# Kernel tuning notes

Hardware: AMD Instinct MI355X
Metric: run time of the kernel (lower is better)

## Reference

```python
import jax, jax.numpy as jnp
import numpy as np

EMBED_DIM = 1024
NUM_HEADS = 16
HEAD_DIM = EMBED_DIM // NUM_HEADS
SCALE = float(np.sqrt(HEAD_DIM))


def setup_inputs() -> dict:
    key = jax.random.key(0)
    ks = jax.random.split(key, 5)
    B, S, D = 4, 2048, EMBED_DIM
    lim_qkv = 1.0 / np.sqrt(D)
    lim_out = 1.0 / np.sqrt(D)
    return {
        "x": jax.random.normal(ks[0], (B, S, D), dtype=jnp.float32),
        "qkv_w": jax.random.uniform(ks[1], (3 * D, D), jnp.float32, -lim_qkv, lim_qkv),
        "qkv_b": jax.random.uniform(ks[2], (3 * D,), jnp.float32, -lim_qkv, lim_qkv),
        "out_w": jax.random.uniform(ks[3], (D, D), jnp.float32, -lim_out, lim_out),
        "out_b": jax.random.uniform(ks[4], (D,), jnp.float32, -lim_out, lim_out),
    }


def reference(x, qkv_w, qkv_b, out_w, out_b):
    B, S, D = x.shape
    H, Hd = NUM_HEADS, HEAD_DIM
    # qkv projection (torch Linear: x @ W.T + b)
    qkv = x @ qkv_w.T + qkv_b                      # [B, S, 3D]
    qkv = qkv.reshape(B, S, 3, H, Hd)
    q = jnp.transpose(qkv[:, :, 0], (0, 2, 1, 3))  # [B, H, S, Hd]
    k = jnp.transpose(qkv[:, :, 1], (0, 2, 1, 3))
    v = jnp.transpose(qkv[:, :, 2], (0, 2, 1, 3))
    attn = jnp.einsum("bhqd,bhkd->bhqk", q, k) / SCALE  # [B, H, S, S]
    attn = jax.nn.softmax(attn, axis=-1)
    out = jnp.einsum("bhqk,bhkd->bhqd", attn, v)        # [B, H, S, Hd]
    out = jnp.transpose(out, (0, 2, 1, 3)).reshape(B, S, D)
    return out @ out_w.T + out_b
```

## Files before the change

kernel.cpp:

```cpp
#include <hip/hip_runtime.h>

typedef unsigned short u16;
typedef __bf16 bf16x8 __attribute__((ext_vector_type(8)));
typedef __bf16 bf16x4 __attribute__((ext_vector_type(4)));
typedef float f32x4 __attribute__((ext_vector_type(4)));
typedef float f32x16 __attribute__((ext_vector_type(16)));
typedef unsigned u32x2 __attribute__((ext_vector_type(2)));

#define AS1 __attribute__((address_space(1)))
#define AS3 __attribute__((address_space(3)))

__device__ __forceinline__ void gload_lds16(const void* g, void* l) {
  __builtin_amdgcn_global_load_lds((const AS1 void*)g, (AS3 void*)l, 16, 0, 0);
}

__device__ __forceinline__ f32x4 mfma16(bf16x8 a, bf16x8 b, f32x4 c) {
  return __builtin_amdgcn_mfma_f32_16x16x32_bf16(a, b, c, 0, 0, 0);
}
__device__ __forceinline__ f32x16 mfma32(bf16x8 a, bf16x8 b, f32x16 c) {
  return __builtin_amdgcn_mfma_f32_32x32x16_bf16(a, b, c, 0, 0, 0);
}

#define QSCALE 0.18033688011112042f

__global__ __launch_bounds__(256) void k_f32_to_bf16(const float* __restrict__ src,
                                                     u16* __restrict__ dst, int n) {
  int i = (blockIdx.x * 256 + threadIdx.x) * 8;
  if (i >= n) return;
  float4 a = *(const float4*)(src + i);
  float4 b = *(const float4*)(src + i + 4);
  union { bf16x8 v; uint4 q; } o;
  o.v[0] = (__bf16)a.x; o.v[1] = (__bf16)a.y; o.v[2] = (__bf16)a.z; o.v[3] = (__bf16)a.w;
  o.v[4] = (__bf16)b.x; o.v[5] = (__bf16)b.y; o.v[6] = (__bf16)b.z; o.v[7] = (__bf16)b.w;
  *(uint4*)(dst + i) = o.q;
}

template <int MODE>
__global__ __launch_bounds__(256) void k_gemm_bt(
    const u16* __restrict__ A, const u16* __restrict__ W,
    const float* __restrict__ bias, float* __restrict__ Cout,
    u16* __restrict__ Qo, u16* __restrict__ Ko, u16* __restrict__ Vo,
    int M, int N, int K) {
  __shared__ __align__(16) u16 As[128 * 64];
  __shared__ __align__(16) u16 Bs[128 * 64];
  const int t = threadIdx.x;
  const int m0 = blockIdx.y * 128;
  const int n0 = blockIdx.x * 128;
  const int lane = t & 63;
  const int w = t >> 6;
  const int lr = lane & 15;
  const int hi = lane >> 4;
  const int wm = (w >> 1) * 64;
  const int wn = (w & 1) * 64;

  f32x4 acc[4][4] = {};

  const u16* aptr = A + (size_t)(m0 + (t >> 3)) * K + (t & 7) * 8;
  const u16* wptr = W + (size_t)(n0 + (t >> 3)) * K + (t & 7) * 8;

  for (int kt = 0; kt < K; kt += 64) {
#pragma unroll
    for (int i = 0; i < 4; i++)
      gload_lds16(aptr + (size_t)i * 32 * K + kt, As + i * 2048 + t * 8);
#pragma unroll
    for (int i = 0; i < 4; i++)
      gload_lds16(wptr + (size_t)i * 32 * K + kt, Bs + i * 2048 + t * 8);
    __syncthreads();
#pragma unroll
    for (int kk = 0; kk < 64; kk += 32) {
      bf16x8 af[4], bfr[4];
#pragma unroll
      for (int mi = 0; mi < 4; mi++)
        af[mi] = *(const bf16x8*)(As + (wm + mi * 16 + lr) * 64 + kk + hi * 8);
#pragma unroll
      for (int ni = 0; ni < 4; ni++)
        bfr[ni] = *(const bf16x8*)(Bs + (wn + ni * 16 + lr) * 64 + kk + hi * 8);
#pragma unroll
      for (int mi = 0; mi < 4; mi++)
#pragma unroll
        for (int ni = 0; ni < 4; ni++)
          acc[mi][ni] = mfma16(af[mi], bfr[ni], acc[mi][ni]);
    }
    __syncthreads();
  }

  float bv[4];
#pragma unroll
  for (int ni = 0; ni < 4; ni++) bv[ni] = bias[n0 + wn + ni * 16 + lr];

  if (MODE == 0) {
#pragma unroll
    for (int mi = 0; mi < 4; mi++)
#pragma unroll
      for (int j = 0; j < 4; j++) {
        int m = m0 + wm + mi * 16 + hi * 4 + j;
#pragma unroll
        for (int ni = 0; ni < 4; ni++)
          Cout[(size_t)m * N + n0 + wn + ni * 16 + lr] = acc[mi][ni][j] + bv[ni];
      }
  } else {
    const int bb = m0 >> 11;
    const int sb0 = (m0 & 2047) + wm;
#pragma unroll
    for (int ni = 0; ni < 4; ni++) {
      int n = n0 + wn + ni * 16 + lr;
      int which = n >> 10;
      int h = (n >> 6) & 15;
      int hd = n & 63;
      if (which == 2) {
        u16* dst = Vo + ((size_t)((bb * 16 + h) * 64 + hd)) * 2048;
#pragma unroll
        for (int mi = 0; mi < 4; mi++) {
          int sb = sb0 + mi * 16 + hi * 4;
          bf16x4 pk;
#pragma unroll
          for (int j = 0; j < 4; j++) pk[j] = (__bf16)(acc[mi][ni][j] + bv[ni]);
          *(bf16x4*)(dst + sb) = pk;
        }
      } else {
        const float scl = (which == 0) ? QSCALE : 1.0f;
        u16* dst = ((which == 0) ? Qo : Ko) + (size_t)(bb * 16 + h) * 2048 * 64 + hd;
#pragma unroll
        for (int mi = 0; mi < 4; mi++)
#pragma unroll
          for (int j = 0; j < 4; j++) {
            int s = sb0 + mi * 16 + hi * 4 + j;
            union { __bf16 b; u16 u; } cv;
            cv.b = (__bf16)((acc[mi][ni][j] + bv[ni]) * scl);
            dst[(size_t)s * 64] = cv.u;
          }
      }
    }
  }
}

__global__ __launch_bounds__(256, 4) void k_attn(const u16* __restrict__ Q,
                                                 const u16* __restrict__ K,
                                                 const u16* __restrict__ Vt,
                                                 u16* __restrict__ ctx) {
  __shared__ __align__(16) u16 Ks[2][64 * 64];
  __shared__ __align__(16) u16 Vs[2][64 * 64];

  const int t = threadIdx.x;
  const int lane = t & 63;
  const int w = t >> 6;
  const int r31 = lane & 31;
  const int hw = lane >> 5;

  const int bid = blockIdx.x;
  const int nb = (bid & 7) * 128 + (bid >> 3);
  const int bh = nb >> 4;
  const int q0 = (nb & 15) * 128;

  const u16* qp = Q + (size_t)bh * 2048 * 64;
  const u16* kp = K + (size_t)bh * 2048 * 64;
  const u16* vp = Vt + (size_t)bh * 64 * 2048;

  const int tu = (t & 15) ^ (t >> 4);
  const int srow = (tu >> 3) * 32 + (t >> 4);
  const int scol = (tu & 7) * 8;

#pragma unroll
  for (int i = 0; i < 2; i++)
    gload_lds16(kp + (size_t)(srow + i * 16) * 64 + scol, Ks[0] + i * 2048 + t * 8);
#pragma unroll
  for (int i = 0; i < 2; i++)
    gload_lds16(vp + (size_t)(srow + i * 16) * 2048 + scol, Vs[0] + i * 2048 + t * 8);

  bf16x8 aq[4];
  const u16* qrow = qp + (size_t)(q0 + w * 32 + r31) * 64 + hw * 8;
#pragma unroll
  for (int kd = 0; kd < 4; kd++) aq[kd] = *(const bf16x8*)(qrow + kd * 16);

  bf16x8 ones;
#pragma unroll
  for (int e = 0; e < 8; e++) ones[e] = (__bf16)1.0f;

  asm volatile("s_waitcnt vmcnt(0)" ::: "memory");
  __builtin_amdgcn_sched_barrier(0);
  __builtin_amdgcn_s_barrier();
  __builtin_amdgcn_sched_barrier(0);

  f32x16 o0 = {}, o1 = {}, l_acc = {};

  for (int kt = 0; kt < 32; kt++) {
    const int cur = kt & 1;
    if (kt + 1 < 32) {
      u16* kd_ = Ks[cur ^ 1];
      u16* vd_ = Vs[cur ^ 1];
#pragma unroll
      for (int i = 0; i < 2; i++)
        gload_lds16(kp + (size_t)((kt + 1) * 64 + srow + i * 16) * 64 + scol,
                    kd_ + i * 2048 + t * 8);
#pragma unroll
      for (int i = 0; i < 2; i++)
        gload_lds16(vp + (size_t)(srow + i * 16) * 2048 + (kt + 1) * 64 + scol,
                    vd_ + i * 2048 + t * 8);
      asm volatile("s_waitcnt vmcnt(4)" ::: "memory");
    } else {
      asm volatile("s_waitcnt vmcnt(0)" ::: "memory");
    }
    __builtin_amdgcn_sched_barrier(0);
    __builtin_amdgcn_s_barrier();
    __builtin_amdgcn_sched_barrier(0);

    const u16* kb = Ks[cur];
    const u16* vb = Vs[cur];

    f32x16 s0 = {}, s1 = {};
#pragma unroll
    for (int kd = 0; kd < 4; kd++) {
      int sl0 = (((kd * 2 + hw) ^ (r31 & 15)) << 3);
      int sl1 = (((8 + kd * 2 + hw) ^ (r31 & 15)) << 3);
      bf16x8 ka0 = *(const bf16x8*)(kb + r31 * 128 + sl0);
      bf16x8 ka1 = *(const bf16x8*)(kb + r31 * 128 + sl1);
      s0 = mfma32(ka0, aq[kd], s0);
      s1 = mfma32(ka1, aq[kd], s1);
    }

#pragma unroll
    for (int e = 0; e < 16; e++) {
      s0[e] = __builtin_amdgcn_exp2f(s0[e]);
      s1[e] = __builtin_amdgcn_exp2f(s1[e]);
    }

#pragma unroll
    for (int tile = 0; tile < 2; tile++) {
      f32x16 st = tile ? s1 : s0;
      unsigned pk[8];
#pragma unroll
      for (int p = 0; p < 8; p++) {
        union { __bf16 h[2]; unsigned u; } cv;
        cv.h[0] = (__bf16)st[2 * p];
        cv.h[1] = (__bf16)st[2 * p + 1];
        pk[p] = cv.u;
      }
#pragma unroll
      for (int c = 0; c < 2; c++) {
        u32x2 ra = __builtin_amdgcn_permlane32_swap(pk[4 * c], pk[4 * c + 2], false, false);
        u32x2 rb = __builtin_amdgcn_permlane32_swap(pk[4 * c + 1], pk[4 * c + 3], false, false);
        union { unsigned u[4]; bf16x8 v; } pf;
        pf.u[0] = ra[0]; pf.u[1] = rb[0]; pf.u[2] = ra[1]; pf.u[3] = rb[1];
        const int kap = tile * 2 + c;
        int slv0 = (((kap * 2 + hw) ^ (r31 & 15)) << 3);
        int slv1 = (((8 + kap * 2 + hw) ^ (r31 & 15)) << 3);
        bf16x8 v0 = *(const bf16x8*)(vb + r31 * 128 + slv0);
        bf16x8 v1 = *(const bf16x8*)(vb + r31 * 128 + slv1);
        o0 = mfma32(v0, pf.v, o0);
        o1 = mfma32(v1, pf.v, o1);
        l_acc = mfma32(ones, pf.v, l_acc);
      }
    }
    __builtin_amdgcn_sched_barrier(0);
    __builtin_amdgcn_s_barrier();
  }

  const int bb = bh >> 4, h = bh & 15;
  const float inv = 1.0f / l_acc[0];
  const size_t base = (size_t)(bb * 2048 + q0 + w * 32 + r31) * 1024 + h * 64;
#pragma unroll
  for (int g = 0; g < 4; g++) {
    bf16x4 p0, p1;
#pragma unroll
    for (int j = 0; j < 4; j++) {
      p0[j] = (__bf16)(o0[g * 4 + j] * inv);
      p1[j] = (__bf16)(o1[g * 4 + j] * inv);
    }
    *(bf16x4*)(ctx + base + g * 8 + hw * 4) = p0;
    *(bf16x4*)(ctx + base + 32 + g * 8 + hw * 4) = p1;
  }
}

extern "C" void kernel_launch(void* const* d_in, const int* in_sizes, int n_in,
                              void* d_out, int out_size, void* d_ws, size_t ws_size,
                              hipStream_t stream) {
  const float* x = (const float*)d_in[0];
  const float* qkv_w = (const float*)d_in[1];
  const float* qkv_b = (const float*)d_in[2];
  const float* out_w = (const float*)d_in[3];
  const float* out_b = (const float*)d_in[4];
  float* out = (float*)d_out;
  char* ws = (char*)d_ws;

  u16* xb    = (u16*)(ws + 0);
  u16* wqkvb = (u16*)(ws + 16777216);
  u16* wob   = (u16*)(ws + 23068672);
  u16* Qb    = (u16*)(ws + 25165824);
  u16* Kb    = (u16*)(ws + 41943040);
  u16* Vtb   = (u16*)(ws + 58720256);
  u16* ctx   = xb;

  k_f32_to_bf16<<<4096, 256, 0, stream>>>(x, xb, 8388608);
  k_f32_to_bf16<<<1536, 256, 0, stream>>>(qkv_w, wqkvb, 3145728);
  k_f32_to_bf16<<<512, 256, 0, stream>>>(out_w, wob, 1048576);

  k_gemm_bt<1><<<dim3(24, 64), 256, 0, stream>>>(xb, wqkvb, qkv_b, nullptr,
                                                 Qb, Kb, Vtb, 8192, 3072, 1024);
  k_attn<<<1024, 256, 0, stream>>>(Qb, Kb, Vtb, ctx);
  k_gemm_bt<0><<<dim3(8, 64), 256, 0, stream>>>(ctx, wob, out_b, out,
                                                nullptr, nullptr, nullptr,
                                                8192, 1024, 1024);
}
```

Measured before the change: 223.2 us.

## Process two query tiles per wave in attention to reuse K/V fragments

Each attention block now covers 256 queries (64 per wave, split into two 32-row tiles) rather than 128, so every K and V fragment loaded from LDS feeds twice as many MFMAs, and the grid halves to 512 blocks. The softmax denominator now comes from VALU row sums plus a cross-half shuffle, replacing the extra MFMA against a ones vector. The loop barrier moves to the top with a full vmcnt(0) wait before the next prefetch is issued. The costs are higher register pressure (launch bounds drop from 4 to 2 blocks per SM), fewer blocks to spread across CUs, and less overlap between the prefetch and the wait.

Result: no change. 220.8 us (-1.1%).

```diff
diff --git a/kernel.cpp b/kernel.cpp
--- a/kernel.cpp
+++ b/kernel.cpp
@@ -19,6 +19,33 @@
 }
 __device__ __forceinline__ f32x16 mfma32(bf16x8 a, bf16x8 b, f32x16 c) {
   return __builtin_amdgcn_mfma_f32_32x32x16_bf16(a, b, c, 0, 0, 0);
+}
+
+__device__ __forceinline__ float rsum16(f32x16 v) {
+  float a0 = v[0] + v[1],  a1 = v[2] + v[3];
+  float a2 = v[4] + v[5],  a3 = v[6] + v[7];
+  float a4 = v[8] + v[9],  a5 = v[10] + v[11];
+  float a6 = v[12] + v[13], a7 = v[14] + v[15];
+  return ((a0 + a1) + (a2 + a3)) + ((a4 + a5) + (a6 + a7));
+}
+
+__device__ __forceinline__ void pack2(const f32x16& st, bf16x8& f0, bf16x8& f1) {
+  unsigned pk[8];
+#pragma unroll
+  for (int p = 0; p < 8; p++) {
+    union { __bf16 h[2]; unsigned u; } cv;
+    cv.h[0] = (__bf16)st[2 * p];
+    cv.h[1] = (__bf16)st[2 * p + 1];
+    pk[p] = cv.u;
+  }
+  u32x2 ra = __builtin_amdgcn_permlane32_swap(pk[0], pk[2], false, false);
+  u32x2 rb = __builtin_amdgcn_permlane32_swap(pk[1], pk[3], false, false);
+  u32x2 rc = __builtin_amdgcn_permlane32_swap(pk[4], pk[6], false, false);
+  u32x2 rd = __builtin_amdgcn_permlane32_swap(pk[5], pk[7], false, false);
+  union { unsigned u[4]; bf16x8 v; } a, b;
+  a.u[0] = ra[0]; a.u[1] = rb[0]; a.u[2] = ra[1]; a.u[3] = rb[1];
+  b.u[0] = rc[0]; b.u[1] = rd[0]; b.u[2] = rc[1]; b.u[3] = rd[1];
+  f0 = a.v; f1 = b.v;
 }
 
 #define QSCALE 0.18033688011112042f
@@ -134,7 +161,7 @@
   }
 }
 
-__global__ __launch_bounds__(256, 4) void k_attn(const u16* __restrict__ Q,
+__global__ __launch_bounds__(256, 2) void k_attn(const u16* __restrict__ Q,
                                                  const u16* __restrict__ K,
                                                  const u16* __restrict__ Vt,
                                                  u16* __restrict__ ctx) {
@@ -148,9 +175,9 @@
   const int hw = lane >> 5;
 
   const int bid = blockIdx.x;
-  const int nb = (bid & 7) * 128 + (bid >> 3);
-  const int bh = nb >> 4;
-  const int q0 = (nb & 15) * 128;
+  const int nb = (bid & 7) * 64 + (bid >> 3);
+  const int bh = nb >> 3;
+  const int q0 = (nb & 7) * 256;
 
   const u16* qp = Q + (size_t)bh * 2048 * 64;
   const u16* kp = K + (size_t)bh * 2048 * 64;
@@ -167,24 +194,27 @@
   for (int i = 0; i < 2; i++)
     gload_lds16(vp + (size_t)(srow + i * 16) * 2048 + scol, Vs[0] + i * 2048 + t * 8);
 
-  bf16x8 aq[4];
-  const u16* qrow = qp + (size_t)(q0 + w * 32 + r31) * 64 + hw * 8;
-#pragma unroll
-  for (int kd = 0; kd < 4; kd++) aq[kd] = *(const bf16x8*)(qrow + kd * 16);
-
-  bf16x8 ones;
-#pragma unroll
-  for (int e = 0; e < 8; e++) ones[e] = (__bf16)1.0f;
-
-  asm volatile("s_waitcnt vmcnt(0)" ::: "memory");
-  __builtin_amdgcn_sched_barrier(0);
-  __builtin_amdgcn_s_barrier();
-  __builtin_amdgcn_sched_barrier(0);
-
-  f32x16 o0 = {}, o1 = {}, l_acc = {};
+  bf16x8 aq0[4], aq1[4];
+  {
+    const u16* qr0 = qp + (size_t)(q0 + w * 64 + r31) * 64 + hw * 8;
+    const u16* qr1 = qr0 + 32 * 64;
+#pragma unroll
+    for (int kd = 0; kd < 4; kd++) {
+      aq0[kd] = *(const bf16x8*)(qr0 + kd * 16);
+      aq1[kd] = *(const bf16x8*)(qr1 + kd * 16);
+    }
+  }
+
+  f32x16 o00 = {}, o01 = {}, o10 = {}, o11 = {};
+  float l0 = 0.f, l1 = 0.f;
 
   for (int kt = 0; kt < 32; kt++) {
     const int cur = kt & 1;
+    asm volatile("s_waitcnt vmcnt(0)" ::: "memory");
+    __builtin_amdgcn_sched_barrier(0);
+    __builtin_amdgcn_s_barrier();
+    __builtin_amdgcn_sched_barrier(0);
+
     if (kt + 1 < 32) {
       u16* kd_ = Ks[cur ^ 1];
       u16* vd_ = Vs[cur ^ 1];
@@ -196,78 +226,97 @@
       for (int i = 0; i < 2; i++)
         gload_lds16(vp + (size_t)(srow + i * 16) * 2048 + (kt + 1) * 64 + scol,
                     vd_ + i * 2048 + t * 8);
-      asm volatile("s_waitcnt vmcnt(4)" ::: "memory");
-    } else {
-      asm volatile("s_waitcnt vmcnt(0)" ::: "memory");
-    }
-    __builtin_amdgcn_sched_barrier(0);
-    __builtin_amdgcn_s_barrier();
-    __builtin_amdgcn_sched_barrier(0);
+    }
 
     const u16* kb = Ks[cur];
     const u16* vb = Vs[cur];
 
-    f32x16 s0 = {}, s1 = {};
+    bf16x8 kfA[4], kfB[4];
 #pragma unroll
     for (int kd = 0; kd < 4; kd++) {
-      int sl0 = (((kd * 2 + hw) ^ (r31 & 15)) << 3);
-      int sl1 = (((8 + kd * 2 + hw) ^ (r31 & 15)) << 3);
-      bf16x8 ka0 = *(const bf16x8*)(kb + r31 * 128 + sl0);
-      bf16x8 ka1 = *(const bf16x8*)(kb + r31 * 128 + sl1);
-      s0 = mfma32(ka0, aq[kd], s0);
-      s1 = mfma32(ka1, aq[kd], s1);
-    }
-
-#pragma unroll
-    for (int e = 0; e < 16; e++) {
-      s0[e] = __builtin_amdgcn_exp2f(s0[e]);
-      s1[e] = __builtin_amdgcn_exp2f(s1[e]);
-    }
-
-#pragma unroll
-    for (int tile = 0; tile < 2; tile++) {
-      f32x16 st = tile ? s1 : s0;
-      unsigned pk[8];
-#pragma unroll
-      for (int p = 0; p < 8; p++) {
-        union { __bf16 h[2]; unsigned u; } cv;
-        cv.h[0] = (__bf16)st[2 * p];
-        cv.h[1] = (__bf16)st[2 * p + 1];
-        pk[p] = cv.u;
-      }
-#pragma unroll
-      for (int c = 0; c < 2; c++) {
-        u32x2 ra = __builtin_amdgcn_permlane32_swap(pk[4 * c], pk[4 * c + 2], false, false);
-        u32x2 rb = __builtin_amdgcn_permlane32_swap(pk[4 * c + 1], pk[4 * c + 3], false, false);
-        union { unsigned u[4]; bf16x8 v; } pf;
-        pf.u[0] = ra[0]; pf.u[1] = rb[0]; pf.u[2] = ra[1]; pf.u[3] = rb[1];
-        const int kap = tile * 2 + c;
-        int slv0 = (((kap * 2 + hw) ^ (r31 & 15)) << 3);
-        int slv1 = (((8 + kap * 2 + hw) ^ (r31 & 15)) << 3);
-        bf16x8 v0 = *(const bf16x8*)(vb + r31 * 128 + slv0);
-        bf16x8 v1 = *(const bf16x8*)(vb + r31 * 128 + slv1);
-        o0 = mfma32(v0, pf.v, o0);
-        o1 = mfma32(v1, pf.v, o1);
-        l_acc = mfma32(ones, pf.v, l_acc);
-      }
-    }
-    __builtin_amdgcn_sched_barrier(0);
-    __builtin_amdgcn_s_barrier();
+      kfA[kd] = *(const bf16x8*)(kb + r31 * 128 + (((kd * 2 + hw) ^ (r31 & 15)) << 3));
+      kfB[kd] = *(const bf16x8*)(kb + r31 * 128 + (((8 + kd * 2 + hw) ^ (r31 & 15)) << 3));
+    }
+
+    bf16x8 pf0[4], pf1[4];
+    {
+      f32x16 sA = {}, sB = {};
+#pragma unroll
+      for (int kd = 0; kd < 4; kd++) {
+        sA = mfma32(kfA[kd], aq0[kd], sA);
+        sB = mfma32(kfB[kd], aq0[kd], sB);
+      }
+#pragma unroll
+      for (int e = 0; e < 16; e++) {
+        sA[e] = __builtin_amdgcn_exp2f(sA[e]);
+        sB[e] = __builtin_amdgcn_exp2f(sB[e]);
+      }
+      float rs = rsum16(sA) + rsum16(sB);
+      rs += __shfl_xor(rs, 32);
+      l0 += rs;
+      pack2(sA, pf0[0], pf0[1]);
+      pack2(sB, pf0[2], pf0[3]);
+    }
+    {
+      f32x16 sA = {}, sB = {};
+#pragma unroll
+      for (int kd = 0; kd < 4; kd++) {
+        sA = mfma32(kfA[kd], aq1[kd], sA);
+        sB = mfma32(kfB[kd], aq1[kd], sB);
+      }
+#pragma unroll
+      for (int e = 0; e < 16; e++) {
+        sA[e] = __builtin_amdgcn_exp2f(sA[e]);
+        sB[e] = __builtin_amdgcn_exp2f(sB[e]);
+      }
+      float rs = rsum16(sA) + rsum16(sB);
+      rs += __shfl_xor(rs, 32);
+      l1 += rs;
+      pack2(sA, pf1[0], pf1[1]);
+      pack2(sB, pf1[2], pf1[3]);
+    }
+
+#pragma unroll
+    for (int kap = 0; kap < 4; kap++) {
+      bf16x8 v0 = *(const bf16x8*)(vb + r31 * 128 + (((kap * 2 + hw) ^ (r31 & 15)) << 3));
+      bf16x8 v1 = *(const bf16x8*)(vb + r31 * 128 + (((8 + kap * 2 + hw) ^ (r31 & 15)) << 3));
+      o00 = mfma32(v0, pf0[kap], o00);
+      o10 = mfma32(v0, pf1[kap], o10);
+      o01 = mfma32(v1, pf0[kap], o01);
+      o11 = mfma32(v1, pf1[kap], o11);
+    }
   }
 
   const int bb = bh >> 4, h = bh & 15;
-  const float inv = 1.0f / l_acc[0];
-  const size_t base = (size_t)(bb * 2048 + q0 + w * 32 + r31) * 1024 + h * 64;
-#pragma unroll
-  for (int g = 0; g < 4; g++) {
-    bf16x4 p0, p1;
-#pragma unroll
-    for (int j = 0; j < 4; j++) {
-      p0[j] = (__bf16)(o0[g * 4 + j] * inv);
-      p1[j] = (__bf16)(o1[g * 4 + j] * inv);
-    }
-    *(bf16x4*)(ctx + base + g * 8 + hw * 4) = p0;
-    *(bf16x4*)(ctx + base + 32 + g * 8 + hw * 4) = p1;
+  {
+    const float inv = 1.0f / l0;
+    const size_t base = (size_t)(bb * 2048 + q0 + w * 64 + r31) * 1024 + h * 64;
+#pragma unroll
+    for (int g = 0; g < 4; g++) {
+      bf16x4 p0, p1;
+#pragma unroll
+      for (int j = 0; j < 4; j++) {
+        p0[j] = (__bf16)(o00[g * 4 + j] * inv);
+        p1[j] = (__bf16)(o01[g * 4 + j] * inv);
+      }
+      *(bf16x4*)(ctx + base + g * 8 + hw * 4) = p0;
+      *(bf16x4*)(ctx + base + 32 + g * 8 + hw * 4) = p1;
+    }
+  }
+  {
+    const float inv = 1.0f / l1;
+    const size_t base = (size_t)(bb * 2048 + q0 + w * 64 + 32 + r31) * 1024 + h * 64;
+#pragma unroll
+    for (int g = 0; g < 4; g++) {
+      bf16x4 p0, p1;
+#pragma unroll
+      for (int j = 0; j < 4; j++) {
+        p0[j] = (__bf16)(o10[g * 4 + j] * inv);
+        p1[j] = (__bf16)(o11[g * 4 + j] * inv);
+      }
+      *(bf16x4*)(ctx + base + g * 8 + hw * 4) = p0;
+      *(bf16x4*)(ctx + base + 32 + g * 8 + hw * 4) = p1;
+    }
   }
 }
 
@@ -296,7 +345,7 @@
 
   k_gemm_bt<1><<<dim3(24, 64), 256, 0, stream>>>(xb, wqkvb, qkv_b, nullptr,
                                                  Qb, Kb, Vtb, 8192, 3072, 1024);
-  k_attn<<<1024, 256, 0, stream>>>(Qb, Kb, Vtb, ctx);
+  k_attn<<<512, 256, 0, stream>>>(Qb, Kb, Vtb, ctx);
   k_gemm_bt<0><<<dim3(8, 64), 256, 0, stream>>>(ctx, wob, out_b, out,
                                                 nullptr, nullptr, nullptr,
                                                 8192, 1024, 1024);
```
